# Kernel tuning notes

Measured on AMD Instinct MI355X. Metric: run time of the kernel, lower is better.

Reference implementation:

```python
import jax, jax.numpy as jnp
import numpy as np

GRID = (128, 128, 16)
VSIZE = 0.5  # voxel_size, pc_range = 0
B, V, N, K, C = 2, 100000, 8192, 8, 64
EPS = 1e-5
OFFSETS = [(dx, dy, dz) for dx in (-1, 0, 1) for dy in (-1, 0, 1) for dz in (-1, 0, 1)]


def setup_inputs() -> dict:
    key = jax.random.key(0)
    ks = jax.random.split(key, 8)
    world = jnp.array([GRID[0] * VSIZE, GRID[1] * VSIZE, GRID[2] * VSIZE], jnp.float32)
    keypoints = jax.random.uniform(ks[0], (B, N, K, 3), jnp.float32) * world
    query_feature = jax.random.normal(ks[1], (B, N, C), jnp.float32)
    voxel_feature = jax.random.normal(ks[2], (B, V, C), jnp.float32)
    # unique voxel coords per batch (hash-map / sparse-tensor semantics)
    cells = GRID[0] * GRID[1] * GRID[2]
    perm = jax.vmap(lambda k: jax.random.permutation(k, cells)[:V])(jax.random.split(ks[3], B))
    x = perm // (GRID[1] * GRID[2])
    rem = perm % (GRID[1] * GRID[2])
    voxel_coords = jnp.stack([x, rem // GRID[2], rem % GRID[2]], -1).astype(jnp.int32)
    W1 = jax.random.normal(ks[4], (27, C, C), jnp.float32) * 0.05
    W2 = jax.random.normal(ks[5], (27, C, C), jnp.float32) * 0.05
    proj_W = jax.random.normal(ks[6], (C, C), jnp.float32) / np.sqrt(C).astype(np.float32)
    proj_b = jnp.zeros((C,), jnp.float32)
    return dict(keypoints=keypoints, query_feature=query_feature,
                voxel_feature=voxel_feature, voxel_coords=voxel_coords,
                W1=W1, bn1_gamma=jnp.ones((C,), jnp.float32), bn1_beta=jnp.zeros((C,), jnp.float32),
                W2=W2, bn2_gamma=jnp.ones((C,), jnp.float32), bn2_beta=jnp.zeros((C,), jnp.float32),
                proj_W=proj_W, proj_b=proj_b)


def _subm_conv(feats, grid, cb, cxyz, W):
    # feats: (M, C); grid: (B, X, Y, Z) int32 flat row index or -1; W: (27, Cin, Cout)
    out = jnp.zeros((feats.shape[0], W.shape[-1]), feats.dtype)
    for k, (dx, dy, dz) in enumerate(OFFSETS):
        nx, ny, nz = cxyz[:, 0] + dx, cxyz[:, 1] + dy, cxyz[:, 2] + dz
        valid = (nx >= 0) & (nx < GRID[0]) & (ny >= 0) & (ny < GRID[1]) & (nz >= 0) & (nz < GRID[2])
        nidx = grid[cb, jnp.clip(nx, 0, GRID[0] - 1), jnp.clip(ny, 0, GRID[1] - 1), jnp.clip(nz, 0, GRID[2] - 1)]
        nidx = jnp.where(valid, nidx, -1)
        nf = jnp.where((nidx >= 0)[:, None], feats[jnp.maximum(nidx, 0)], jnp.zeros((), feats.dtype))
        out = out + nf @ W[k]
    return out


def _bn_relu(x, gamma, beta):
    # BatchNorm1d in training mode: batch stats (biased var), then ReLU
    mu = x.mean(0)
    var = jnp.var(x, axis=0)
    return jax.nn.relu((x - mu) * jax.lax.rsqrt(var + EPS) * gamma + beta)


def reference(keypoints, query_feature, voxel_feature, voxel_coords,
              W1, bn1_gamma, bn1_beta, W2, bn2_gamma, bn2_beta, proj_W, proj_b):
    coords = voxel_coords.reshape(-1, 3).astype(jnp.int32)
    cb = jnp.repeat(jnp.arange(B, dtype=jnp.int32), V)
    # dense grid hash: cell -> flat voxel row, -1 if empty (replaces Python dict)
    grid = jnp.full((B,) + GRID, -1, jnp.int32)
    grid = grid.at[cb, coords[:, 0], coords[:, 1], coords[:, 2]].set(jnp.arange(B * V, dtype=jnp.int32))
    feats = voxel_feature.reshape(-1, C)
    feats = _bn_relu(_subm_conv(feats, grid, cb, coords, W1), bn1_gamma, bn1_beta)
    feats = _bn_relu(_subm_conv(feats, grid, cb, coords, W2), bn2_gamma, bn2_beta)
    # quantize keypoints (pc_range = 0, trunc == floor since coords >= 0)
    q = (keypoints / VSIZE).astype(jnp.int32)
    q = jnp.clip(q, 0, jnp.array(GRID, jnp.int32) - 1)  # (B, N, K, 3)
    bidx = jnp.arange(B, dtype=jnp.int32)[:, None, None]
    idx = grid[bidx, q[..., 0], q[..., 1], q[..., 2]]   # (B, N, K); -1 -> fallback row 0
    sampled = feats[jnp.maximum(idx, 0)]                 # (B, N, K, C)
    fused = (sampled.mean(2) + query_feature) @ proj_W.T + proj_b
    voxel_indices = jnp.concatenate(
        [jnp.broadcast_to(bidx[..., None], (B, N, K, 1)), q], axis=-1).reshape(-1, 4)
    return fused, voxel_indices
```

## Files before the change

kernel.cpp:

```cpp
#include <hip/hip_runtime.h>
#include <hip/hip_bf16.h>
#include <math.h>

#define GX 128
#define GY 128
#define GZ 16
#define CELLS (GX*GY*GZ)
#define NCELLT (NB*CELLS)
#define NB 2
#define NV 100000
#define NM (NB*NV)
#define NN 8192
#define NK 8
#define NC 64
#define EPSV 1e-5f
#define TM 128
#define NTILE 196
#define NBLK (8*NTILE)
#define NMT (NBLK*TM)
#define KPH 4

typedef __attribute__((ext_vector_type(8))) short short8;
typedef __attribute__((ext_vector_type(4))) float floatx4;

__device__ __forceinline__ float bf2f(unsigned short u) {
    unsigned int x = ((unsigned int)u) << 16;
    return __builtin_bit_cast(float, x);
}
__device__ __forceinline__ unsigned short f2bf(float f) {
    unsigned int u = __builtin_bit_cast(unsigned int, f);
    return (unsigned short)((u + 0x7fffu + ((u >> 16) & 1u)) >> 16);
}

__global__ void k_init(int* __restrict__ grid, float* __restrict__ stats,
                       unsigned short* __restrict__ featA) {
    int i = blockIdx.x * 256 + threadIdx.x;
    if (i < NCELLT) grid[i] = -1;
    else if (i < NCELLT + 512) stats[i - NCELLT] = 0.f;
    else if (i < NCELLT + 512 + 64) featA[(size_t)NM * 64 + (i - NCELLT - 512)] = 0;
}

__global__ void k_scatter(const int* __restrict__ coords, int* __restrict__ grid) {
    int gid = blockIdx.x * 256 + threadIdx.x;
    if (gid >= NM) return;
    int b = (gid >= NV) ? 1 : 0;
    int x = coords[gid * 3 + 0];
    int y = coords[gid * 3 + 1];
    int z = coords[gid * 3 + 2];
    grid[((b * GX + x) * GY + y) * GZ + z] = gid;
}

__global__ void k_count(const int* __restrict__ grid, int* __restrict__ bcnt) {
    __shared__ int wt[4];
    int t = threadIdx.x;
    int occ = (grid[blockIdx.x * 256 + t] >= 0) ? 1 : 0;
    int w = t >> 6;
    unsigned long long m = __ballot(occ);
    if ((t & 63) == 0) wt[w] = __popcll(m);
    __syncthreads();
    if (t == 0) bcnt[blockIdx.x] = wt[0] + wt[1] + wt[2] + wt[3];
}

__global__ void k_scan2048(const int* __restrict__ bcnt, int* __restrict__ boff) {
    __shared__ int s[256];
    int t = threadIdx.x;
    int v[8], sum = 0;
    #pragma unroll
    for (int j = 0; j < 8; ++j) {
        int x = bcnt[t * 8 + j];
        v[j] = sum;
        sum += x;
    }
    s[t] = sum;
    __syncthreads();
    for (int off = 1; off < 256; off <<= 1) {
        int x = (t >= off) ? s[t - off] : 0;
        __syncthreads();
        s[t] += x;
        __syncthreads();
    }
    int excl = s[t] - sum;
    #pragma unroll
    for (int j = 0; j < 8; ++j) boff[t * 8 + j] = excl + v[j];
}

__global__ void k_assign(const int* __restrict__ gold, const int* __restrict__ boff,
                         int* __restrict__ gnew, int* __restrict__ perm,
                         int* __restrict__ scell) {
    __shared__ int wt[4];
    int t = threadIdx.x;
    int cell = blockIdx.x * 256 + t;
    int old = gold[cell];
    int occ = (old >= 0) ? 1 : 0;
    int w = t >> 6, lane = t & 63;
    unsigned long long m = __ballot(occ);
    int lp = __popcll(m & ((1ULL << lane) - 1ULL));
    if (lane == 63) wt[w] = lp + occ;
    __syncthreads();
    int wbase = 0;
    #pragma unroll
    for (int j = 0; j < 4; ++j) if (j < w) wbase += wt[j];
    int nid = boff[blockIdx.x] + wbase + lp;
    if (occ) {
        gnew[cell] = nid;
        perm[nid] = old;
        scell[nid] = cell;
    } else {
        gnew[cell] = -1;
    }
}

__global__ void k_nbr(const int* __restrict__ scell, const int* __restrict__ gnew,
                      const int* __restrict__ vcoords,
                      int* __restrict__ nid, int* __restrict__ fbp) {
    if (blockIdx.x == 0 && threadIdx.x == 0) {
        int cell0 = (vcoords[0] * GY + vcoords[1]) * GZ + vcoords[2];
        fbp[0] = gnew[cell0];
    }
    int m = blockIdx.x * 256 + threadIdx.x;
    if (m >= NMT) return;
    int cell = (m < NM) ? scell[m] : -1;
    int x = 0, y = 0, z = 0;
    if (cell >= 0) { x = (cell >> 11) & 127; y = (cell >> 4) & 127; z = cell & 15; }
    #pragma unroll
    for (int k = 0; k < 28; ++k) {
        int ni = NM;
        if (k < 27 && cell >= 0) {
            int dx = k / 9 - 1, dy = (k / 3) % 3 - 1, dz = k % 3 - 1;
            int nx = x + dx, ny = y + dy, nz = z + dz;
            if (nx >= 0 && nx < GX && ny >= 0 && ny < GY && nz >= 0 && nz < GZ) {
                int g = gnew[cell + dx * (GY * GZ) + dy * GZ + dz];
                ni = (g < 0) ? NM : g;
            }
        }
        nid[(size_t)k * NMT + m] = ni;
    }
}

__global__ void k_prep(const float* __restrict__ W1, const float* __restrict__ W2,
                       const float* __restrict__ vfeat, const int* __restrict__ perm,
                       unsigned short* __restrict__ Wt1, unsigned short* __restrict__ Wt2,
                       unsigned short* __restrict__ featA) {
    int bid = blockIdx.x;
    if (bid < 56) {
        int e = bid * 256 + threadIdx.x;
        int lane = e & 63;
        int fr = (e >> 6) & 7;
        int k = e >> 9;
        int ct = fr >> 1, ks = fr & 1;
        int quad = lane >> 4, n16 = lane & 15;
        int co = ct * 16 + n16;
        #pragma unroll
        for (int j = 0; j < 8; ++j) {
            int ci = ks * 32 + quad * 8 + j;
            unsigned short w1 = 0, w2 = 0;
            if (k < 27) {
                w1 = f2bf(W1[(k << 12) + ci * 64 + co]);
                w2 = f2bf(W2[(k << 12) + ci * 64 + co]);
            }
            Wt1[(size_t)e * 8 + j] = w1;
            Wt2[(size_t)e * 8 + j] = w2;
        }
    } else {
        int i = (bid - 56) * 256 + threadIdx.x;
        if (i >= NM * 8) return;
        int mrow = i >> 3, part = i & 7;
        int src = perm[mrow];
        const float4* s = (const float4*)(vfeat + (size_t)src * 64 + part * 8);
        float4 a = s[0], b = s[1];
        ushort4 lo, hi;
        lo.x = f2bf(a.x); lo.y = f2bf(a.y); lo.z = f2bf(a.z); lo.w = f2bf(a.w);
        hi.x = f2bf(b.x); hi.y = f2bf(b.y); hi.z = f2bf(b.z); hi.w = f2bf(b.w);
        ushort4* d = (ushort4*)(featA + (size_t)mrow * 64 + part * 8);
        d[0] = lo; d[1] = hi;
    }
}

__global__ __launch_bounds__(256, 3) void k_conv(
    const unsigned short* __restrict__ feats, const int* __restrict__ nid,
    const unsigned short* __restrict__ Wt,
    unsigned short* __restrict__ out, float* __restrict__ gsum, float* __restrict__ gsq)
{
    __shared__ unsigned short s_b[KPH * 4096];

    int tid = threadIdx.x;
    int bid = blockIdx.x;
    int tile = (bid & 7) * NTILE + (bid >> 3);
    int m0 = tile * TM;

    int w = tid >> 6, lane = tid & 63;
    int quad = lane >> 4, n16 = lane & 15;
    const unsigned short* fq = feats + quad * 8;
    const int* nbase = nid + m0 + w * 32 + n16;

    short8 afr[3][4];
    int nidr[2][KPH][2];

    auto issueA = [&](const int* nr, short8* af) {
        #pragma unroll
        for (int rt = 0; rt < 2; ++rt) {
            const unsigned short* r0 = fq + (size_t)nr[rt] * 64;
            af[rt * 2 + 0] = *(const short8*)(r0);
            af[rt * 2 + 1] = *(const short8*)(r0 + 32);
        }
    };

    floatx4 acc[2][4];
    #pragma unroll
    for (int rt = 0; rt < 2; ++rt)
        #pragma unroll
        for (int ct = 0; ct < 4; ++ct)
            acc[rt][ct] = (floatx4){0.f, 0.f, 0.f, 0.f};

    const uint4* wt4 = (const uint4*)Wt;

    #pragma unroll
    for (int j = 0; j < KPH; ++j) {
        nidr[0][j][0] = nbase[(size_t)j * NMT];
        nidr[0][j][1] = nbase[(size_t)j * NMT + 16];
    }

    for (int ph = 0; ph < 7; ++ph) {
        int k0 = ph * KPH;
        int cur = ph & 1;
        __syncthreads();
        #pragma unroll
        for (int i = 0; i < KPH * 2; ++i)
            ((uint4*)s_b)[i * 256 + tid] = wt4[(size_t)k0 * 512 + i * 256 + tid];
        if (ph < 6) {
            #pragma unroll
            for (int j = 0; j < KPH; ++j) {
                nidr[cur ^ 1][j][0] = nbase[(size_t)(k0 + KPH + j) * NMT];
                nidr[cur ^ 1][j][1] = nbase[(size_t)(k0 + KPH + j) * NMT + 16];
            }
        }
        issueA(nidr[cur][0], afr[0]);
        issueA(nidr[cur][1], afr[1]);
        __syncthreads();

        #pragma unroll
        for (int j = 0; j < KPH; ++j) {
            if (j + 2 < KPH) issueA(nidr[cur][j + 2], afr[(j + 2) % 3]);
            __builtin_amdgcn_sched_barrier(0);

            const unsigned short* bb = s_b + j * 4096;
            short8 bfr[8];
            #pragma unroll
            for (int fr = 0; fr < 8; ++fr)
                bfr[fr] = *(const short8*)(bb + fr * 512 + lane * 8);

            const short8* ac = afr[j % 3];
            #pragma unroll
            for (int ks = 0; ks < 2; ++ks)
                #pragma unroll
                for (int rt = 0; rt < 2; ++rt)
                    #pragma unroll
                    for (int ct = 0; ct < 4; ++ct)
                        acc[rt][ct] = __builtin_amdgcn_mfma_f32_16x16x32_bf16(
                            ac[rt * 2 + ks], bfr[ct * 2 + ks], acc[rt][ct], 0, 0, 0);
            __builtin_amdgcn_sched_barrier(0);
        }
    }

    #pragma unroll
    for (int rt = 0; rt < 2; ++rt) {
        int rbase = m0 + w * 32 + rt * 16 + quad * 4;
        #pragma unroll
        for (int rg = 0; rg < 4; ++rg) {
            int m = rbase + rg;
            if (m < NM) {
                #pragma unroll
                for (int ct = 0; ct < 4; ++ct)
                    out[(size_t)m * 64 + ct * 16 + n16] = f2bf(acc[rt][ct][rg]);
            }
        }
    }

    float ps[4], pq[4];
    #pragma unroll
    for (int ct = 0; ct < 4; ++ct) { ps[ct] = 0.f; pq[ct] = 0.f; }
    #pragma unroll
    for (int rt = 0; rt < 2; ++rt)
        #pragma unroll
        for (int ct = 0; ct < 4; ++ct)
            #pragma unroll
            for (int rg = 0; rg < 4; ++rg) {
                float v = acc[rt][ct][rg];
                ps[ct] += v;
                pq[ct] += v * v;
            }
    #pragma unroll
    for (int ct = 0; ct < 4; ++ct) {
        ps[ct] += __shfl_xor(ps[ct], 16);
        ps[ct] += __shfl_xor(ps[ct], 32);
        pq[ct] += __shfl_xor(pq[ct], 16);
        pq[ct] += __shfl_xor(pq[ct], 32);
    }
    __syncthreads();
    float* red = (float*)s_b;
    if (lane < 16) {
        #pragma unroll
        for (int ct = 0; ct < 4; ++ct) {
            red[w * 64 + ct * 16 + n16]       = ps[ct];
            red[256 + w * 64 + ct * 16 + n16] = pq[ct];
        }
    }
    __syncthreads();
    if (tid < 64) {
        float ts = 0.f, tq = 0.f;
        #pragma unroll
        for (int ww = 0; ww < 4; ++ww) {
            ts += red[ww * 64 + tid];
            tq += red[256 + ww * 64 + tid];
        }
        atomicAdd(gsum + tid, ts);
        atomicAdd(gsq + tid, tq);
    }
}

__global__ void k_bnapply(const unsigned short* __restrict__ in,
                          const float* __restrict__ gsum, const float* __restrict__ gsq,
                          const float* __restrict__ gamma, const float* __restrict__ beta,
                          unsigned short* __restrict__ out) {
    int i = blockIdx.x * 256 + threadIdx.x;
    if (i >= NM * 8) return;
    int c8 = (i & 7) * 8;
    float scv[8], shv[8];
    #pragma unroll
    for (int jj = 0; jj < 8; ++jj) {
        int c = c8 + jj;
        float mu = gsum[c] * (1.f / NM);
        float var = gsq[c] * (1.f / NM) - mu * mu;
        float s = gamma[c] * rsqrtf(var + EPSV);
        scv[jj] = s;
        shv[jj] = beta[c] - mu * s;
    }
    uint4 v = ((const uint4*)in)[i];
    unsigned int vv[4] = {v.x, v.y, v.z, v.w};
    unsigned int oo[4];
    #pragma unroll
    for (int j = 0; j < 4; ++j) {
        float lo = bf2f((unsigned short)(vv[j] & 0xffffu));
        float hi = bf2f((unsigned short)(vv[j] >> 16));
        lo = fmaxf(lo * scv[j * 2]     + shv[j * 2],     0.f);
        hi = fmaxf(hi * scv[j * 2 + 1] + shv[j * 2 + 1], 0.f);
        oo[j] = (unsigned int)f2bf(lo) | ((unsigned int)f2bf(hi) << 16);
    }
    uint4 o = {oo[0], oo[1], oo[2], oo[3]};
    ((uint4*)out)[i] = o;
}

__global__ __launch_bounds__(256) void k_sample(
    const float* __restrict__ kp, const float* __restrict__ query,
    const unsigned short* __restrict__ conv2,
    const float* __restrict__ gsum2, const float* __restrict__ gsq2,
    const float* __restrict__ g2, const float* __restrict__ b2,
    const int* __restrict__ grid, const int* __restrict__ fbp,
    const float* __restrict__ projW, const float* __restrict__ projB,
    float* __restrict__ out_fused, float* __restrict__ out_vi)
{
    __shared__ float s_pw[64 * 65];
    __shared__ float s_mean[4][64];
    __shared__ int   s_idx[4][8];

    int tid = threadIdx.x;
    for (int e = tid; e < 4096; e += 256) {
        int co = e >> 6, c = e & 63;
        s_pw[co * 65 + c] = projW[e];
    }

    int w = tid >> 6, lane = tid & 63;
    int row = blockIdx.x * 4 + w;
    int b = row >> 13;
    float mu = gsum2[lane] * (1.f / NM);
    float var = gsq2[lane] * (1.f / NM) - mu * mu;
    float sc = g2[lane] * rsqrtf(var + EPSV);
    float sh = b2[lane] - mu * sc;
    int fb = fbp[0];
    __syncthreads();

    if (lane < 8) {
        int kk = lane;
        const float* kpp = kp + ((size_t)row * 8 + kk) * 3;
        int qx = min(max((int)(kpp[0] * 2.0f), 0), GX - 1);
        int qy = min(max((int)(kpp[1] * 2.0f), 0), GY - 1);
        int qz = min(max((int)(kpp[2] * 2.0f), 0), GZ - 1);
        s_idx[w][kk] = grid[((b * GX + qx) * GY + qy) * GZ + qz];
        float4 vi = make_float4((float)b, (float)qx, (float)qy, (float)qz);
        *(float4*)(out_vi + ((size_t)row * 8 + kk) * 4) = vi;
    }
    __syncthreads();

    float acc = 0.f;
    #pragma unroll
    for (int kk = 0; kk < 8; ++kk) {
        int gi = s_idx[w][kk];
        gi = gi < 0 ? fb : gi;
        float v = bf2f(conv2[(size_t)gi * 64 + lane]);
        acc += fmaxf(v * sc + sh, 0.f);
    }
    float mean = acc * 0.125f + query[(size_t)row * 64 + lane];
    s_mean[w][lane] = mean;
    __syncthreads();

    float f = projB[lane];
    const float* pwr = s_pw + lane * 65;
    const float* mv = s_mean[w];
    #pragma unroll 8
    for (int c = 0; c < 64; ++c) f += mv[c] * pwr[c];
    out_fused[(size_t)row * 64 + lane] = f;
}

extern "C" void kernel_launch(void* const* d_in, const int* in_sizes, int n_in,
                              void* d_out, int out_size, void* d_ws, size_t ws_size,
                              hipStream_t stream) {
    const float* keypoints = (const float*)d_in[0];
    const float* query     = (const float*)d_in[1];
    const float* vfeat     = (const float*)d_in[2];
    const int*   vcoords   = (const int*)d_in[3];
    const float* W1        = (const float*)d_in[4];
    const float* g1        = (const float*)d_in[5];
    const float* b1        = (const float*)d_in[6];
    const float* W2        = (const float*)d_in[7];
    const float* g2        = (const float*)d_in[8];
    const float* b2        = (const float*)d_in[9];
    const float* pW        = (const float*)d_in[10];
    const float* pb        = (const float*)d_in[11];

    char* ws = (char*)d_ws;
    int*            gold  = (int*)ws;
    int*            gnew  = (int*)(ws + 2097152);
    float*          stats = (float*)(ws + 4194304);
    int*            fbp   = (int*)(ws + 4196352);
    int*            bcnt  = (int*)(ws + 4196608);
    int*            boff  = (int*)(ws + 4204800);
    int*            perm  = (int*)(ws + 4212992);
    int*            scell = (int*)(ws + 5012992);
    unsigned short* Wt1   = (unsigned short*)(ws + 5812992);
    unsigned short* Wt2   = (unsigned short*)(ws + 6042368);
    unsigned short* featA = (unsigned short*)(ws + 6271744);
    int*            nidt  = (int*)(ws + 31872000);
    unsigned short* convo = (unsigned short*)(ws + 54350848);

    float* sum1 = stats,       *sq1 = stats + 64;
    float* sum2 = stats + 256, *sq2 = stats + 320;

    int initN = NCELLT + 512 + 64;
    k_init<<<(initN + 255) / 256, 256, 0, stream>>>(gold, stats, featA);
    k_scatter<<<(NM + 255) / 256, 256, 0, stream>>>(vcoords, gold);

    k_count<<<NCELLT / 256, 256, 0, stream>>>(gold, bcnt);
    k_scan2048<<<1, 256, 0, stream>>>(bcnt, boff);
    k_assign<<<NCELLT / 256, 256, 0, stream>>>(gold, boff, gnew, perm, scell);
    k_nbr<<<NMT / 256, 256, 0, stream>>>(scell, gnew, vcoords, nidt, fbp);

    k_prep<<<56 + (NM * 8 + 255) / 256, 256, 0, stream>>>(W1, W2, vfeat, perm,
                                                          Wt1, Wt2, featA);

    k_conv<<<NBLK, 256, 0, stream>>>(featA, nidt, Wt1, convo, sum1, sq1);
    k_bnapply<<<(NM * 8 + 255) / 256, 256, 0, stream>>>(convo, sum1, sq1, g1, b1, featA);

    k_conv<<<NBLK, 256, 0, stream>>>(featA, nidt, Wt2, convo, sum2, sq2);

    float* out_fused = (float*)d_out;
    float* out_vi = out_fused + (size_t)NB * NN * NC;
    k_sample<<<(NB * NN) / 4, 256, 0, stream>>>(keypoints, query, convo, sum2, sq2, g2, b2,
                                                gnew, fbp, pW, pb, out_fused, out_vi);
}
```

Before: 325.0 us.

## Make sparse conv persistent with XCD-aware atomic tile work-stealing

The conv kernel now launches a fixed pool of 512 persistent blocks. Each block pulls 128-row tiles from per-XCD atomic counters, starting with its own XCD (read from the hardware register) and stealing from others once its queue is empty. BN statistics are accumulated across all tiles and reduced once per block, which cuts the number of global atomic flushes. In exchange it adds an atomic and two barriers per tile, and lowers the launch-bounds occupancy hint from 3 to 2; the counters rely on the stats region being zeroed by the init kernel.

```diff
diff --git a/kernel.cpp b/kernel.cpp
--- a/kernel.cpp
+++ b/kernel.cpp
@@ -16,9 +16,9 @@
 #define EPSV 1e-5f
 #define TM 128
 #define NTILE 196
-#define NBLK (8*NTILE)
-#define NMT (NBLK*TM)
+#define NMT (8*NTILE*TM)
 #define KPH 4
+#define NPBLK 512
 
 typedef __attribute__((ext_vector_type(8))) short short8;
 typedef __attribute__((ext_vector_type(4))) float floatx4;
@@ -176,22 +176,23 @@
     }
 }
 
-__global__ __launch_bounds__(256, 3) void k_conv(
+__global__ __launch_bounds__(256, 2) void k_conv(
     const unsigned short* __restrict__ feats, const int* __restrict__ nid,
-    const unsigned short* __restrict__ Wt,
+    const unsigned short* __restrict__ Wt, int* __restrict__ ctr,
     unsigned short* __restrict__ out, float* __restrict__ gsum, float* __restrict__ gsq)
 {
     __shared__ unsigned short s_b[KPH * 4096];
+    __shared__ int s_tile;
 
     int tid = threadIdx.x;
-    int bid = blockIdx.x;
-    int tile = (bid & 7) * NTILE + (bid >> 3);
-    int m0 = tile * TM;
-
     int w = tid >> 6, lane = tid & 63;
     int quad = lane >> 4, n16 = lane & 15;
     const unsigned short* fq = feats + quad * 8;
-    const int* nbase = nid + m0 + w * 32 + n16;
+    const uint4* wt4 = (const uint4*)Wt;
+
+    int myxcd;
+    asm volatile("s_getreg_b32 %0, hwreg(HW_REG_XCC_ID)" : "=s"(myxcd));
+    myxcd &= 7;
 
     short8 afr[3][4];
     int nidr[2][KPH][2];
@@ -205,90 +206,107 @@
         }
     };
 
-    floatx4 acc[2][4];
-    #pragma unroll
-    for (int rt = 0; rt < 2; ++rt)
-        #pragma unroll
-        for (int ct = 0; ct < 4; ++ct)
-            acc[rt][ct] = (floatx4){0.f, 0.f, 0.f, 0.f};
-
-    const uint4* wt4 = (const uint4*)Wt;
-
-    #pragma unroll
-    for (int j = 0; j < KPH; ++j) {
-        nidr[0][j][0] = nbase[(size_t)j * NMT];
-        nidr[0][j][1] = nbase[(size_t)j * NMT + 16];
-    }
-
-    for (int ph = 0; ph < 7; ++ph) {
-        int k0 = ph * KPH;
-        int cur = ph & 1;
+    float ps[4] = {0.f, 0.f, 0.f, 0.f}, pq[4] = {0.f, 0.f, 0.f, 0.f};
+
+    for (;;) {
+        if (tid == 0) {
+            int t = -1;
+            #pragma unroll
+            for (int xx0 = 0; xx0 < 8; ++xx0) {
+                int xx = (myxcd + xx0) & 7;
+                int v = atomicAdd(ctr + xx, 1);
+                if (v < NTILE) { t = xx * NTILE + v; break; }
+            }
+            s_tile = t;
+        }
         __syncthreads();
-        #pragma unroll
-        for (int i = 0; i < KPH * 2; ++i)
-            ((uint4*)s_b)[i * 256 + tid] = wt4[(size_t)k0 * 512 + i * 256 + tid];
-        if (ph < 6) {
+        int tile = s_tile;
+        if (tile < 0) break;
+        int m0 = tile * TM;
+        const int* nbase = nid + m0 + w * 32 + n16;
+
+        floatx4 acc[2][4];
+        #pragma unroll
+        for (int rt = 0; rt < 2; ++rt)
+            #pragma unroll
+            for (int ct = 0; ct < 4; ++ct)
+                acc[rt][ct] = (floatx4){0.f, 0.f, 0.f, 0.f};
+
+        #pragma unroll
+        for (int j = 0; j < KPH; ++j) {
+            nidr[0][j][0] = nbase[(size_t)j * NMT];
+            nidr[0][j][1] = nbase[(size_t)j * NMT + 16];
+        }
+
+        for (int ph = 0; ph < 7; ++ph) {
+            int k0 = ph * KPH;
+            int cur = ph & 1;
+            __syncthreads();
+            #pragma unroll
+            for (int i = 0; i < KPH * 2; ++i)
+                ((uint4*)s_b)[i * 256 + tid] = wt4[(size_t)k0 * 512 + i * 256 + tid];
+            if (ph < 6) {
+                #pragma unroll
+                for (int j = 0; j < KPH; ++j) {
+                    nidr[cur ^ 1][j][0] = nbase[(size_t)(k0 + KPH + j) * NMT];
+                    nidr[cur ^ 1][j][1] = nbase[(size_t)(k0 + KPH + j) * NMT + 16];
+                }
+            }
+            issueA(nidr[cur][0], afr[0]);
+            issueA(nidr[cur][1], afr[1]);
+            __syncthreads();
+
             #pragma unroll
             for (int j = 0; j < KPH; ++j) {
-                nidr[cur ^ 1][j][0] = nbase[(size_t)(k0 + KPH + j) * NMT];
-                nidr[cur ^ 1][j][1] = nbase[(size_t)(k0 + KPH + j) * NMT + 16];
-            }
-        }
-        issueA(nidr[cur][0], afr[0]);
-        issueA(nidr[cur][1], afr[1]);
-        __syncthreads();
-
-        #pragma unroll
-        for (int j = 0; j < KPH; ++j) {
-            if (j + 2 < KPH) issueA(nidr[cur][j + 2], afr[(j + 2) % 3]);
-            __builtin_amdgcn_sched_barrier(0);
-
-            const unsigned short* bb = s_b + j * 4096;
-            short8 bfr[8];
-            #pragma unroll
-            for (int fr = 0; fr < 8; ++fr)
-                bfr[fr] = *(const short8*)(bb + fr * 512 + lane * 8);
-
-            const short8* ac = afr[j % 3];
-            #pragma unroll
-            for (int ks = 0; ks < 2; ++ks)
+                if (j + 2 < KPH) issueA(nidr[cur][j + 2], afr[(j + 2) % 3]);
+                __builtin_amdgcn_sched_barrier(0);
+
+                const unsigned short* bb = s_b + j * 4096;
+                short8 bfr[8];
                 #pragma unroll
-                for (int rt = 0; rt < 2; ++rt)
+                for (int fr = 0; fr < 8; ++fr)
+                    bfr[fr] = *(const short8*)(bb + fr * 512 + lane * 8);
+
+                const short8* ac = afr[j % 3];
+                #pragma unroll
+                for (int ks = 0; ks < 2; ++ks)
+                    #pragma unroll
+                    for (int rt = 0; rt < 2; ++rt)
+                        #pragma unroll
+                        for (int ct = 0; ct < 4; ++ct)
+                            acc[rt][ct] = __builtin_amdgcn_mfma_f32_16x16x32_bf16(
+                                ac[rt * 2 + ks], bfr[ct * 2 + ks], acc[rt][ct], 0, 0, 0);
+                __builtin_amdgcn_sched_barrier(0);
+            }
+        }
+
+        #pragma unroll
+        for (int rt = 0; rt < 2; ++rt) {
+            int rbase = m0 + w * 32 + rt * 16 + quad * 4;
+            #pragma unroll
+            for (int rg = 0; rg < 4; ++rg) {
+                int m = rbase + rg;
+                if (m < NM) {
                     #pragma unroll
                     for (int ct = 0; ct < 4; ++ct)
-                        acc[rt][ct] = __builtin_amdgcn_mfma_f32_16x16x32_bf16(
-                            ac[rt * 2 + ks], bfr[ct * 2 + ks], acc[rt][ct], 0, 0, 0);
-            __builtin_amdgcn_sched_barrier(0);
-        }
-    }
-
-    #pragma unroll
-    for (int rt = 0; rt < 2; ++rt) {
-        int rbase = m0 + w * 32 + rt * 16 + quad * 4;
-        #pragma unroll
-        for (int rg = 0; rg < 4; ++rg) {
-            int m = rbase + rg;
-            if (m < NM) {
+                        out[(size_t)m * 64 + ct * 16 + n16] = f2bf(acc[rt][ct][rg]);
+                }
+            }
+        }
+
+        #pragma unroll
+        for (int rt = 0; rt < 2; ++rt)
+            #pragma unroll
+            for (int ct = 0; ct < 4; ++ct)
                 #pragma unroll
-                for (int ct = 0; ct < 4; ++ct)
-                    out[(size_t)m * 64 + ct * 16 + n16] = f2bf(acc[rt][ct][rg]);
-            }
-        }
-    }
-
-    float ps[4], pq[4];
-    #pragma unroll
-    for (int ct = 0; ct < 4; ++ct) { ps[ct] = 0.f; pq[ct] = 0.f; }
-    #pragma unroll
-    for (int rt = 0; rt < 2; ++rt)
-        #pragma unroll
-        for (int ct = 0; ct < 4; ++ct)
-            #pragma unroll
-            for (int rg = 0; rg < 4; ++rg) {
-                float v = acc[rt][ct][rg];
-                ps[ct] += v;
-                pq[ct] += v * v;
-            }
+                for (int rg = 0; rg < 4; ++rg) {
+                    float v = acc[rt][ct][rg];
+                    ps[ct] += v;
+                    pq[ct] += v * v;
+                }
+        __syncthreads();
+    }
+
     #pragma unroll
     for (int ct = 0; ct < 4; ++ct) {
         ps[ct] += __shfl_xor(ps[ct], 16);
@@ -444,6 +462,8 @@
 
     float* sum1 = stats,       *sq1 = stats + 64;
     float* sum2 = stats + 256, *sq2 = stats + 320;
+    int*   ctr1 = (int*)(stats + 128);
+    int*   ctr2 = (int*)(stats + 384);
 
     int initN = NCELLT + 512 + 64;
     k_init<<<(initN + 255) / 256, 256, 0, stream>>>(gold, stats, featA);
@@ -457,10 +477,10 @@
     k_prep<<<56 + (NM * 8 + 255) / 256, 256, 0, stream>>>(W1, W2, vfeat, perm,
                                                           Wt1, Wt2, featA);
 
-    k_conv<<<NBLK, 256, 0, stream>>>(featA, nidt, Wt1, convo, sum1, sq1);
+    k_conv<<<NPBLK, 256, 0, stream>>>(featA, nidt, Wt1, ctr1, convo, sum1, sq1);
     k_bnapply<<<(NM * 8 + 255) / 256, 256, 0, stream>>>(convo, sum1, sq1, g1, b1, featA);
 
-    k_conv<<<NBLK, 256, 0, stream>>>(featA, nidt, Wt2, convo, sum2, sq2);
+    k_conv<<<NPBLK, 256, 0, stream>>>(featA, nidt, Wt2, ctr2, convo, sum2, sq2);
 
     float* out_fused = (float*)d_out;
     float* out_vi = out_fused + (size_t)NB * NN * NC;
```

Result: slower. 436.6 us (+34.3%).
